# Kernel tuning notes

Measured on AMD Instinct MI355X. Metric: run time of the kernel, lower is better.

## Reference

```python
import jax, jax.numpy as jnp
import numpy as np

B, L, S, H, E = 2, 2048, 2048, 16, 64


def setup_inputs() -> dict:
    key = jax.random.key(0)
    kq, kk, kv = jax.random.split(key, 3)
    queries = jax.random.normal(kq, (B, L, H, E), dtype=jnp.float32)
    keys = jax.random.normal(kk, (B, S, H, E), dtype=jnp.float32)
    values = jax.random.normal(kv, (B, S, H, E), dtype=jnp.float32)
    attn_mask = jnp.ones((B, 1, L, S), dtype=jnp.float32)  # >0.5 means attend
    return {"queries": queries, "keys": keys, "values": values, "attn_mask": attn_mask}


def reference(queries, keys, values, attn_mask):
    # queries: [B,L,H,E], keys/values: [B,S,H,E], attn_mask broadcastable to [B,H,L,S]
    E_ = queries.shape[-1]
    scale = 1.0 / np.sqrt(E_).astype(np.float32)
    scores = jnp.einsum('blhe,bshe->bhls', queries, keys)  # [B,H,L,S]
    large_negative = jnp.float32(-1e9)
    scores = scores + jnp.where(attn_mask > 0.5, jnp.float32(0.0), large_negative)
    A = jax.nn.softmax(scale * scores, axis=-1)  # dropout p=0.0 -> identity
    V = jnp.einsum('bhls,bshd->bhld', A, values)  # [B,H,L,D]
    return V
```

## Files before the change

### kernel.cpp

```cpp
#include <hip/hip_runtime.h>

typedef float    f32x4 __attribute__((ext_vector_type(4)));
typedef _Float16 f16x2 __attribute__((ext_vector_type(2)));
typedef _Float16 f16x4 __attribute__((ext_vector_type(4)));
typedef _Float16 f16x8 __attribute__((ext_vector_type(8)));
typedef int      i32x4 __attribute__((ext_vector_type(4)));

namespace {
constexpr int B_ = 2, L_ = 2048, S_ = 2048, H_ = 16, E_ = 64;
constexpr int MBLK = 128;
constexpr int NT = 64;
constexpr int NTILES = S_ / NT;

#define SCALE2f 0.1803368801111204f
#define MBIAS2f -1.8033688e8f

constexpr size_t KHOFF = (size_t)1 << 20;
constexpr size_t VHOFF = KHOFF + (size_t)B_ * H_ * S_ * E_ * 2;

__device__ __forceinline__ f16x2 cvt2(float a, float b) {
  return __builtin_bit_cast(f16x2, __builtin_amdgcn_cvt_pkrtz(a, b));
}
__device__ __forceinline__ int pkh(float a, float b) {
  return __builtin_bit_cast(int, __builtin_amdgcn_cvt_pkrtz(a, b));
}
union H8 { f16x8 v; i32x4 i; };
union H4 { f16x4 v; f16x2 h[2]; };

#define GLOAD_LDS16(g, l)                                              \
  __builtin_amdgcn_global_load_lds(                                    \
      (const __attribute__((address_space(1))) void*)(g),              \
      (__attribute__((address_space(3))) void*)(l), 16, 0, 0)
}

extern "C" __global__ __launch_bounds__(256)
void prep_kernel(const float* __restrict__ Kg, const float* __restrict__ Vg,
                 const float* __restrict__ Mg, _Float16* __restrict__ Kh,
                 _Float16* __restrict__ Vh, unsigned long long* __restrict__ Wb) {
  __shared__ _Float16 T[64][72];
  const int bid = blockIdx.x;
  const int t   = threadIdx.x;

  if (bid < 2048) {
    const int idx = bid * 256 + t;
    const int j = idx & 7;
    const int h = (idx >> 3) & (H_ - 1);
    const int s = (idx >> 7) & (S_ - 1);
    const int b = idx >> 18;
    const float* src = Kg + ((((size_t)b * S_ + s) * H_ + h) << 6) + j * 8;
    f32x4 x = *(const f32x4*)src, y = *(const f32x4*)(src + 4);
    i32x4 w = {pkh(x[0], x[1]), pkh(x[2], x[3]), pkh(y[0], y[1]), pkh(y[2], y[3])};
    *(i32x4*)(Kh + ((((size_t)b * H_ + h) * S_ + s) << 6) + j * 8) = w;
  } else if (bid < 4096) {
    const int u = (bid - 2048) * 256 + t;
    const float* src = Mg + (size_t)u * 16;
    unsigned m = 0;
#pragma unroll
    for (int i = 0; i < 4; ++i) {
      f32x4 x = *(const f32x4*)(src + i * 4);
#pragma unroll
      for (int c = 0; c < 4; ++c) m |= (x[c] > 0.5f ? 1u : 0u) << (i * 4 + c);
    }
    ((unsigned short*)Wb)[u] = (unsigned short)m;
  } else {
    const int vb = bid - 4096;
    const int st = vb & 31;
    const int h  = (vb >> 5) & (H_ - 1);
    const int b  = vb >> 9;
    const int sl = t >> 2;
    const int e0 = (t & 3) << 4;
    const float* src = Vg + ((((size_t)b * S_ + st * 64 + sl) * H_ + h) << 6) + e0;
#pragma unroll
    for (int i = 0; i < 4; ++i) {
      f32x4 x = *(const f32x4*)(src + i * 4);
#pragma unroll
      for (int c = 0; c < 4; ++c) T[e0 + i * 4 + c][sl] = (_Float16)x[c];
    }
    __syncthreads();
    const int er = t >> 2;
    const int s0 = (t & 3) << 4;
    _Float16* dst = Vh + (((((size_t)b * H_ + h) << 6) + er) * S_) + st * 64 + s0;
    *(i32x4*)dst       = *(const i32x4*)&T[er][s0];
    *(i32x4*)(dst + 8) = *(const i32x4*)&T[er][s0 + 8];
  }
}

extern "C" __global__ __launch_bounds__(512, 4)
void fattn_kernel(const float* __restrict__ Qg, const _Float16* __restrict__ Kh,
                  const _Float16* __restrict__ Vh, const unsigned long long* __restrict__ Wb,
                  float* __restrict__ Og) {
  __shared__ __align__(16) _Float16 Ks[3][NT][64];
  __shared__ __align__(16) _Float16 Vt[3][E_][64];

  const int tid  = threadIdx.x;
  const int wv   = tid >> 6;
  const int lane = tid & 63;
  const int qd   = lane >> 4;
  const int cl   = lane & 15;
  const int sw   = cl & 7;

  const int bid = blockIdx.x;
  const int qb  = bid >> 5;
  const int bh  = bid & 31;
  const int h   = bh & (H_ - 1);
  const int b   = bh >> 4;

  const int l0 = qb * MBLK + wv * 16;

  f16x8 qf[2];
  {
    const float* qp = Qg + ((((size_t)b * L_ + (l0 + cl)) * H_ + h) << 6);
#pragma unroll
    for (int kb = 0; kb < 2; ++kb) {
      const int e0 = qd * 8 + kb * 32;
      f32x4 x = *(const f32x4*)(qp + e0);
      f32x4 y = *(const f32x4*)(qp + e0 + 4);
      H8 u;
      u.i = (i32x4){pkh(x[0], x[1]), pkh(x[2], x[3]), pkh(y[0], y[1]), pkh(y[2], y[3])};
      qf[kb] = u.v;
    }
  }

  const int rl  = lane >> 3;
  const int gsl = lane & 7;
  const int gsw = gsl ^ rl;
  const _Float16* khb = Kh + ((((size_t)b * H_ + h) * S_) << 6);
  const _Float16* vhb = Vh + ((((size_t)b * H_ + h) << 6) * (size_t)S_);

  const unsigned long long* wbp = Wb + (((size_t)b * L_ + (l0 + cl)) << 5);

  auto dma = [&](int buf, int t) {
    const int r0 = wv * 8;
    const _Float16* ksrc = khb + (((size_t)(t * 64 + r0 + rl)) << 6) + gsw * 8;
    GLOAD_LDS16(ksrc, &Ks[buf][r0][0]);
    const _Float16* vsrc = vhb + (size_t)(r0 + rl) * S_ + t * 64 + gsw * 8;
    GLOAD_LDS16(vsrc, &Vt[buf][r0][0]);
  };

  const f32x4 zero4 = {0.f, 0.f, 0.f, 0.f};
  f32x4 acc[4];
#pragma unroll
  for (int et = 0; et < 4; ++et) acc[et] = zero4;
  f32x4 rs4 = zero4;

  unsigned long long mwcur = wbp[0];
  dma(0, 0);
  asm volatile("" ::: "memory");
  __builtin_amdgcn_sched_barrier(0);
  unsigned long long mwnext = wbp[1];
  dma(1, 1);

  int bc = 0;
  for (int t = 0; t < NTILES; ++t) {
    __builtin_amdgcn_sched_barrier(0);
    if (t < NTILES - 1)
      asm volatile("s_waitcnt vmcnt(3) lgkmcnt(0)" ::: "memory");
    else
      asm volatile("s_waitcnt vmcnt(0) lgkmcnt(0)" ::: "memory");
    __builtin_amdgcn_s_barrier();
    __builtin_amdgcn_sched_barrier(0);

    unsigned long long mwnext2 = 0;
    if (t + 2 < NTILES) {
      int b2 = bc + 2; if (b2 >= 3) b2 -= 3;
      mwnext2 = wbp[t + 2];
      dma(b2, t + 2);
    }

    f32x4 sc[4];
    __builtin_amdgcn_s_setprio(1);
#pragma unroll
    for (int nt = 0; nt < 4; ++nt) {
      const _Float16* krow = &Ks[bc][nt * 16 + cl][0];
      const f16x8 a0 = *(const f16x8*)(krow + ((qd ^ sw) << 3));
      const f16x8 a1 = *(const f16x8*)(krow + (((qd + 4) ^ sw) << 3));
      f32x4 c = zero4;
      c = __builtin_amdgcn_mfma_f32_16x16x32_f16(a0, qf[0], c, 0, 0, 0);
      c = __builtin_amdgcn_mfma_f32_16x16x32_f16(a1, qf[1], c, 0, 0, 0);
      sc[nt] = c;
    }
    __builtin_amdgcn_s_setprio(0);

    f16x4 pa[4];
    if (mwcur == ~0ull) {
#pragma unroll
      for (int nt = 0; nt < 4; ++nt) {
        f32x4 p;
#pragma unroll
        for (int r = 0; r < 4; ++r)
          p[r] = __builtin_amdgcn_exp2f(sc[nt][r] * SCALE2f);
        rs4 += p;
        H4 u;
        u.h[0] = cvt2(p[0], p[1]);
        u.h[1] = cvt2(p[2], p[3]);
        pa[nt] = u.v;
      }
    } else {
      const unsigned lo = (unsigned)mwcur;
      const unsigned hi = (unsigned)(mwcur >> 32);
#pragma unroll
      for (int nt = 0; nt < 4; ++nt) {
        const unsigned shm = ((nt < 2) ? lo : hi) >> ((nt & 1) * 16 + qd * 4);
        f32x4 p;
#pragma unroll
        for (int r = 0; r < 4; ++r) {
          const float bias = (shm & (1u << r)) ? 0.f : MBIAS2f;
          p[r] = __builtin_amdgcn_exp2f(__builtin_fmaf(sc[nt][r], SCALE2f, bias));
        }
        rs4 += p;
        H4 u;
        u.h[0] = cvt2(p[0], p[1]);
        u.h[1] = cvt2(p[2], p[3]);
        pa[nt] = u.v;
      }
    }

    __builtin_amdgcn_s_setprio(1);
#pragma unroll
    for (int nt = 0; nt < 4; ++nt)
#pragma unroll
      for (int et = 0; et < 4; ++et) {
        const _Float16* vrow = &Vt[bc][et * 16 + cl][0];
        const f16x4 bv = *(const f16x4*)(vrow + ((((2 * nt + (qd >> 1)) ^ sw) << 3) + ((qd & 1) << 2)));
        acc[et] = __builtin_amdgcn_mfma_f32_16x16x16f16(pa[nt], bv, acc[et], 0, 0, 0);
      }
    __builtin_amdgcn_s_setprio(0);

    mwcur = mwnext;
    mwnext = mwnext2;
    bc = (bc + 1 == 3) ? 0 : bc + 1;
  }

  {
    float v = rs4[0] + rs4[1] + rs4[2] + rs4[3];
    v += __shfl_xor(v, 16, 64);
    v += __shfl_xor(v, 32, 64);
#pragma unroll
    for (int r = 0; r < 4; ++r) {
      const float invq = 1.0f / __shfl(v, qd * 4 + r, 64);
      const int l = l0 + qd * 4 + r;
      float* op = Og + ((((size_t)b * H_ + h) * L_ + l) << 6) + cl;
#pragma unroll
      for (int et = 0; et < 4; ++et) op[et * 16] = acc[et][r] * invq;
    }
  }
}

extern "C" void kernel_launch(void* const* d_in, const int* in_sizes, int n_in,
                              void* d_out, int out_size, void* d_ws, size_t ws_size,
                              hipStream_t stream) {
  const float* Q = (const float*)d_in[0];
  const float* K = (const float*)d_in[1];
  const float* V = (const float*)d_in[2];
  const float* M = (const float*)d_in[3];
  float* O = (float*)d_out;
  unsigned long long* Wb = (unsigned long long*)d_ws;
  _Float16* Khp = (_Float16*)((char*)d_ws + KHOFF);
  _Float16* Vhp = (_Float16*)((char*)d_ws + VHOFF);

  hipLaunchKernelGGL(prep_kernel, dim3(5120), dim3(256), 0, stream, K, V, M, Khp, Vhp, Wb);
  hipLaunchKernelGGL(fattn_kernel, dim3(B_ * H_ * (L_ / MBLK)), dim3(512), 0, stream,
                     Q, Khp, Vhp, Wb, O);
}
```

Baseline: 168.3 us.

## Split key range across two blocks with combine pass and software-pipelined PV

Splits the key/value sequence into two halves handled by separate blocks when workspace allows, writing unnormalized partial outputs and row sums, then adds a combine kernel that sums them and normalizes. This doubles the grid from 512 blocks to raise occupancy and CU utilization. The loop also moves to double-buffer style prefetch with a plain __syncthreads(), and defers the PV MFMA by one tile so it overlaps with the next QK and exp. The softmax scale is folded into Q, and launch bounds are raised to 6 blocks per CU. In exchange it adds an extra kernel launch plus global round-trips for the partial outputs, and it depends on the workspace size.

Result: slower. 191.6 us (+13.8%).

```diff
diff --git a/kernel.cpp b/kernel.cpp
--- a/kernel.cpp
+++ b/kernel.cpp
@@ -15,8 +15,12 @@
 #define SCALE2f 0.1803368801111204f
 #define MBIAS2f -1.8033688e8f
 
-constexpr size_t KHOFF = (size_t)1 << 20;
-constexpr size_t VHOFF = KHOFF + (size_t)B_ * H_ * S_ * E_ * 2;
+constexpr size_t KHOFF  = (size_t)1 << 20;
+constexpr size_t VHOFF  = KHOFF + (size_t)B_ * H_ * S_ * E_ * 2;
+constexpr size_t POOFF  = (size_t)17 << 20;
+constexpr size_t RS0OFF = (size_t)33 << 20;
+constexpr size_t RS1OFF = RS0OFF + ((size_t)256 << 10);
+constexpr size_t WSNEED = RS1OFF + ((size_t)256 << 10);
 
 __device__ __forceinline__ f16x2 cvt2(float a, float b) {
   return __builtin_bit_cast(f16x2, __builtin_amdgcn_cvt_pkrtz(a, b));
@@ -85,10 +89,11 @@
   }
 }
 
-extern "C" __global__ __launch_bounds__(512, 4)
+extern "C" __global__ __launch_bounds__(512, 6)
 void fattn_kernel(const float* __restrict__ Qg, const _Float16* __restrict__ Kh,
                   const _Float16* __restrict__ Vh, const unsigned long long* __restrict__ Wb,
-                  float* __restrict__ Og) {
+                  float* __restrict__ Og, float* __restrict__ PO1,
+                  float* __restrict__ RS0, float* __restrict__ RS1, int nsg) {
   __shared__ __align__(16) _Float16 Ks[3][NT][64];
   __shared__ __align__(16) _Float16 Vt[3][E_][64];
 
@@ -99,11 +104,15 @@
   const int cl   = lane & 15;
   const int sw   = cl & 7;
 
-  const int bid = blockIdx.x;
-  const int qb  = bid >> 5;
-  const int bh  = bid & 31;
-  const int h   = bh & (H_ - 1);
-  const int b   = bh >> 4;
+  const int bid  = blockIdx.x;
+  const int bh   = bid & 31;
+  const int rest = bid >> 5;
+  const int sg   = rest & (nsg - 1);
+  const int qb   = (nsg == 2) ? (rest >> 1) : rest;
+  const int h    = bh & (H_ - 1);
+  const int b    = bh >> 4;
+  const int nts  = (nsg == 2) ? (NTILES / 2) : NTILES;
+  const int ts0  = sg * nts;
 
   const int l0 = qb * MBLK + wv * 16;
 
@@ -115,6 +124,8 @@
       const int e0 = qd * 8 + kb * 32;
       f32x4 x = *(const f32x4*)(qp + e0);
       f32x4 y = *(const f32x4*)(qp + e0 + 4);
+      x *= SCALE2f;
+      y *= SCALE2f;
       H8 u;
       u.i = (i32x4){pkh(x[0], x[1]), pkh(x[2], x[3]), pkh(y[0], y[1]), pkh(y[2], y[3])};
       qf[kb] = u.v;
@@ -127,13 +138,14 @@
   const _Float16* khb = Kh + ((((size_t)b * H_ + h) * S_) << 6);
   const _Float16* vhb = Vh + ((((size_t)b * H_ + h) << 6) * (size_t)S_);
 
-  const unsigned long long* wbp = Wb + (((size_t)b * L_ + (l0 + cl)) << 5);
+  const unsigned long long* wbp = Wb + (((size_t)b * L_ + (l0 + cl)) << 5) + ts0;
 
   auto dma = [&](int buf, int t) {
+    const int ts = ts0 + t;
     const int r0 = wv * 8;
-    const _Float16* ksrc = khb + (((size_t)(t * 64 + r0 + rl)) << 6) + gsw * 8;
+    const _Float16* ksrc = khb + (((size_t)(ts * 64 + r0 + rl)) << 6) + gsw * 8;
     GLOAD_LDS16(ksrc, &Ks[buf][r0][0]);
-    const _Float16* vsrc = vhb + (size_t)(r0 + rl) * S_ + t * 64 + gsw * 8;
+    const _Float16* vsrc = vhb + (size_t)(r0 + rl) * S_ + ts * 64 + gsw * 8;
     GLOAD_LDS16(vsrc, &Vt[buf][r0][0]);
   };
 
@@ -142,33 +154,22 @@
 #pragma unroll
   for (int et = 0; et < 4; ++et) acc[et] = zero4;
   f32x4 rs4 = zero4;
-
+  f16x4 pa[4];
+
+  dma(0, 0);
   unsigned long long mwcur = wbp[0];
-  dma(0, 0);
-  asm volatile("" ::: "memory");
-  __builtin_amdgcn_sched_barrier(0);
-  unsigned long long mwnext = wbp[1];
-  dma(1, 1);
 
   int bc = 0;
-  for (int t = 0; t < NTILES; ++t) {
-    __builtin_amdgcn_sched_barrier(0);
-    if (t < NTILES - 1)
-      asm volatile("s_waitcnt vmcnt(3) lgkmcnt(0)" ::: "memory");
-    else
-      asm volatile("s_waitcnt vmcnt(0) lgkmcnt(0)" ::: "memory");
-    __builtin_amdgcn_s_barrier();
-    __builtin_amdgcn_sched_barrier(0);
-
-    unsigned long long mwnext2 = 0;
-    if (t + 2 < NTILES) {
-      int b2 = bc + 2; if (b2 >= 3) b2 -= 3;
-      mwnext2 = wbp[t + 2];
-      dma(b2, t + 2);
-    }
+  for (int t = 0; t < nts; ++t) {
+    __syncthreads();
+
+    const int bn = (bc == 2) ? 0 : bc + 1;
+    const int bp = (bc == 0) ? 2 : bc - 1;
+    if (t + 1 < nts) dma(bn, t + 1);
+    unsigned long long mwnext = 0;
+    if (t + 1 < nts) mwnext = wbp[t + 1];
 
     f32x4 sc[4];
-    __builtin_amdgcn_s_setprio(1);
 #pragma unroll
     for (int nt = 0; nt < 4; ++nt) {
       const _Float16* krow = &Ks[bc][nt * 16 + cl][0];
@@ -179,16 +180,25 @@
       c = __builtin_amdgcn_mfma_f32_16x16x32_f16(a1, qf[1], c, 0, 0, 0);
       sc[nt] = c;
     }
-    __builtin_amdgcn_s_setprio(0);
-
-    f16x4 pa[4];
+
+    if (t) {
+#pragma unroll
+      for (int nt = 0; nt < 4; ++nt)
+#pragma unroll
+        for (int et = 0; et < 4; ++et) {
+          const _Float16* vrow = &Vt[bp][et * 16 + cl][0];
+          const f16x4 bv = *(const f16x4*)(vrow + ((((2 * nt + (qd >> 1)) ^ sw) << 3) + ((qd & 1) << 2)));
+          acc[et] = __builtin_amdgcn_mfma_f32_16x16x16f16(pa[nt], bv, acc[et], 0, 0, 0);
+        }
+    }
+
     if (mwcur == ~0ull) {
 #pragma unroll
       for (int nt = 0; nt < 4; ++nt) {
         f32x4 p;
 #pragma unroll
         for (int r = 0; r < 4; ++r)
-          p[r] = __builtin_amdgcn_exp2f(sc[nt][r] * SCALE2f);
+          p[r] = __builtin_amdgcn_exp2f(sc[nt][r]);
         rs4 += p;
         H4 u;
         u.h[0] = cvt2(p[0], p[1]);
@@ -205,7 +215,7 @@
 #pragma unroll
         for (int r = 0; r < 4; ++r) {
           const float bias = (shm & (1u << r)) ? 0.f : MBIAS2f;
-          p[r] = __builtin_amdgcn_exp2f(__builtin_fmaf(sc[nt][r], SCALE2f, bias));
+          p[r] = __builtin_amdgcn_exp2f(sc[nt][r] + bias);
         }
         rs4 += p;
         H4 u;
@@ -215,26 +225,27 @@
       }
     }
 
-    __builtin_amdgcn_s_setprio(1);
+    mwcur = mwnext;
+    bc = bn;
+  }
+
+  {
+    const int bl = (nts - 1) % 3;
 #pragma unroll
     for (int nt = 0; nt < 4; ++nt)
 #pragma unroll
       for (int et = 0; et < 4; ++et) {
-        const _Float16* vrow = &Vt[bc][et * 16 + cl][0];
+        const _Float16* vrow = &Vt[bl][et * 16 + cl][0];
         const f16x4 bv = *(const f16x4*)(vrow + ((((2 * nt + (qd >> 1)) ^ sw) << 3) + ((qd & 1) << 2)));
         acc[et] = __builtin_amdgcn_mfma_f32_16x16x16f16(pa[nt], bv, acc[et], 0, 0, 0);
       }
-    __builtin_amdgcn_s_setprio(0);
-
-    mwcur = mwnext;
-    mwnext = mwnext2;
-    bc = (bc + 1 == 3) ? 0 : bc + 1;
-  }
-
-  {
-    float v = rs4[0] + rs4[1] + rs4[2] + rs4[3];
-    v += __shfl_xor(v, 16, 64);
-    v += __shfl_xor(v, 32, 64);
+  }
+
+  float v = rs4[0] + rs4[1] + rs4[2] + rs4[3];
+  v += __shfl_xor(v, 16, 64);
+  v += __shfl_xor(v, 32, 64);
+
+  if (nsg == 1) {
 #pragma unroll
     for (int r = 0; r < 4; ++r) {
       const float invq = 1.0f / __shfl(v, qd * 4 + r, 64);
@@ -243,6 +254,36 @@
 #pragma unroll
       for (int et = 0; et < 4; ++et) op[et * 16] = acc[et][r] * invq;
     }
+  } else {
+    float* po        = sg ? PO1 : Og;
+    float* rsb       = sg ? RS1 : RS0;
+    const size_t rb0 = ((size_t)b * H_ + h) * L_ + l0;
+    if (lane < 16) rsb[rb0 + lane] = v;
+#pragma unroll
+    for (int r = 0; r < 4; ++r) {
+      const int l = l0 + qd * 4 + r;
+      float* op = po + ((((size_t)b * H_ + h) * L_ + l) << 6) + cl;
+#pragma unroll
+      for (int et = 0; et < 4; ++et) op[et * 16] = acc[et][r];
+    }
+  }
+}
+
+extern "C" __global__ __launch_bounds__(256)
+void combine_kernel(float* __restrict__ Og, const float* __restrict__ PO1,
+                    const float* __restrict__ RS0, const float* __restrict__ RS1) {
+  const int idx = blockIdx.x * 256 + threadIdx.x;
+  const int row = idx >> 2;
+  const int c0  = (idx & 3) << 4;
+  const float inv = 1.0f / (RS0[row] + RS1[row]);
+  float* o       = Og  + ((size_t)row << 6) + c0;
+  const float* p = PO1 + ((size_t)row << 6) + c0;
+#pragma unroll
+  for (int i = 0; i < 4; ++i) {
+    f32x4 a = *(const f32x4*)(o + i * 4);
+    f32x4 q = *(const f32x4*)(p + i * 4);
+    f32x4 r = (a + q) * inv;
+    *(f32x4*)(o + i * 4) = r;
   }
 }
 
@@ -257,8 +298,15 @@
   unsigned long long* Wb = (unsigned long long*)d_ws;
   _Float16* Khp = (_Float16*)((char*)d_ws + KHOFF);
   _Float16* Vhp = (_Float16*)((char*)d_ws + VHOFF);
+  float* PO1 = (float*)((char*)d_ws + POOFF);
+  float* RS0 = (float*)((char*)d_ws + RS0OFF);
+  float* RS1 = (float*)((char*)d_ws + RS1OFF);
+
+  const int nsg = (ws_size >= WSNEED) ? 2 : 1;
 
   hipLaunchKernelGGL(prep_kernel, dim3(5120), dim3(256), 0, stream, K, V, M, Khp, Vhp, Wb);
-  hipLaunchKernelGGL(fattn_kernel, dim3(B_ * H_ * (L_ / MBLK)), dim3(512), 0, stream,
-                     Q, Khp, Vhp, Wb, O);
-}
+  hipLaunchKernelGGL(fattn_kernel, dim3(512 * nsg), dim3(512), 0, stream,
+                     Q, Khp, Vhp, Wb, O, PO1, RS0, RS1, nsg);
+  if (nsg == 2)
+    hipLaunchKernelGGL(combine_kernel, dim3(1024), dim3(256), 0, stream, O, PO1, RS0, RS1);
+}
```
